# Kernel optimization log

Hardware: AMD Instinct MI355X
Metric: run time of the kernel (lower is better)

## Reference

```python
import jax, jax.numpy as jnp
import numpy as np

B, N, EMB, H = 16, 1024, 128, 8
INNER = EMB * H  # 1024
EPS = 1e-5


def setup_inputs() -> dict:
    key = jax.random.key(0)
    k1, k2, k3 = jax.random.split(key, 3)
    inputs = jax.random.normal(k1, (B, N, EMB), dtype=jnp.float32)
    ln_gamma = jnp.ones((EMB,), dtype=jnp.float32)
    ln_beta = jnp.zeros((EMB,), dtype=jnp.float32)
    w_qkv = jax.random.normal(k2, (EMB, 3 * INNER), dtype=jnp.float32) * (EMB ** -0.5)
    w_proj = jax.random.normal(k3, (INNER, EMB), dtype=jnp.float32) * (INNER ** -0.5)
    b_proj = jnp.zeros((EMB,), dtype=jnp.float32)
    return {"inputs": inputs, "ln_gamma": ln_gamma, "ln_beta": ln_beta,
            "w_qkv": w_qkv, "w_proj": w_proj, "b_proj": b_proj}


def reference(inputs, ln_gamma, ln_beta, w_qkv, w_proj, b_proj):
    scale = INNER ** -0.5
    # LayerNorm over last dim
    mu = jnp.mean(inputs, axis=-1, keepdims=True)
    var = jnp.var(inputs, axis=-1, keepdims=True)
    x = (inputs - mu) * jax.lax.rsqrt(var + EPS) * ln_gamma + ln_beta
    # QKV projection (no bias)
    qkv = x @ w_qkv                                  # [b, n, 3*inner]
    q, k, v = jnp.split(qkv, 3, axis=-1)             # each [b, n, inner]
    def to_heads(a):
        return a.reshape(B, N, H, EMB).transpose(0, 2, 1, 3)  # [b, h, n, d]
    q, k, v = to_heads(q), to_heads(k), to_heads(v)
    attn = jnp.einsum('bhid,bhjd->bhij', q * scale, k)
    attn = jax.nn.softmax(attn, axis=-1)
    out = jnp.einsum('bhij,bhjd->bhid', attn, v)     # [b, h, n, d]
    out = out.transpose(0, 2, 1, 3).reshape(B, N, INNER)
    return out @ w_proj + b_proj                     # [b, n, emb]
```

## Files before the change

### kernel.cpp

```cpp
#include <hip/hip_runtime.h>
#include <hip/hip_bf16.h>


typedef __attribute__((ext_vector_type(8))) short bf16x8;
typedef __attribute__((ext_vector_type(4))) float f32x4;
typedef __attribute__((ext_vector_type(4))) unsigned int u32x4;

__device__ __forceinline__ unsigned short f2bf(float f) {
  unsigned int u = __float_as_uint(f);
  u += 0x7FFF + ((u >> 16) & 1);
  return (unsigned short)(u >> 16);
}

__device__ __forceinline__ void gll16(const void* g, void* l) {
  __builtin_amdgcn_global_load_lds((const __attribute__((address_space(1))) unsigned int*)g,
                                   (__attribute__((address_space(3))) unsigned int*)l, 16, 0, 0);
}

__global__ __launch_bounds__(256) void k_prep(const float* __restrict__ x,
                                              const float* __restrict__ gamma,
                                              const float* __restrict__ beta,
                                              const float* __restrict__ wqkv,
                                              const float* __restrict__ wproj,
                                              unsigned short* __restrict__ xb,
                                              unsigned short* __restrict__ wqkvT,
                                              unsigned short* __restrict__ wprojT) {
  __shared__ unsigned short T[17152];
  const int bid = blockIdx.x, tid = threadIdx.x;
  if (bid < 4096) {
    int row  = bid * 4 + (tid >> 6);
    int lane = tid & 63;
    float2 v = *reinterpret_cast<const float2*>(x + row * 128 + lane * 2);
    float s = v.x + v.y, ss = v.x * v.x + v.y * v.y;
#pragma unroll
    for (int m = 1; m < 64; m <<= 1) { s += __shfl_xor(s, m); ss += __shfl_xor(ss, m); }
    float mu   = s * (1.0f / 128.0f);
    float var  = ss * (1.0f / 128.0f) - mu * mu;
    float rstd = rsqrtf(var + 1e-5f);
    float2 g  = *reinterpret_cast<const float2*>(gamma + lane * 2);
    float2 be = *reinterpret_cast<const float2*>(beta + lane * 2);
    ushort2 o;
    o.x = f2bf((v.x - mu) * rstd * g.x + be.x);
    o.y = f2bf((v.y - mu) * rstd * g.y + be.y);
    *reinterpret_cast<ushort2*>(xb + row * 128 + lane * 2) = o;
  } else if (bid < 4144) {
    const int n0 = (bid - 4096) * 64;
#pragma unroll
    for (int i = 0; i < 32; i++) {
      int idx = i * 256 + tid;
      int k = idx >> 6, c = idx & 63;
      T[k * 70 + c] = f2bf(wqkv[k * 3072 + n0 + c]);
    }
    __syncthreads();
#pragma unroll
    for (int i = 0; i < 32; i++) {
      int idx = i * 256 + tid;
      int n = idx >> 7, k = idx & 127;
      wqkvT[(n0 + n) * 128 + k] = T[k * 70 + n];
    }
  } else {
    const int k0 = (bid - 4144) * 128;
#pragma unroll
    for (int i = 0; i < 64; i++) {
      int idx = i * 256 + tid;
      int r = idx >> 7, c = idx & 127;
      T[r * 134 + c] = f2bf(wproj[(k0 + r) * 128 + c]);
    }
    __syncthreads();
#pragma unroll
    for (int i = 0; i < 64; i++) {
      int idx = i * 256 + tid;
      int c = idx >> 7, r = idx & 127;
      wprojT[c * 1024 + k0 + r] = T[r * 134 + c];
    }
  }
}

__global__ __launch_bounds__(256) void k_qkv(const unsigned short* __restrict__ xb,
                                             const unsigned short* __restrict__ wt,
                                             unsigned short* __restrict__ qb,
                                             unsigned short* __restrict__ kb,
                                             unsigned short* __restrict__ vtb) {
  __shared__ __align__(16) unsigned short SH[24576];
  unsigned short* Xs = SH;
  unsigned short* Ws = SH + 8192;
  const int m0 = blockIdx.x * 64;
  const int n0 = blockIdx.y * 128;
  const int tid = threadIdx.x, wave = tid >> 6, lane = tid & 63;
  const int lm = lane & 15, lg = lane >> 4;
  const int wr = wave >> 1, wc = wave & 1;

#pragma unroll
  for (int ii = 0; ii < 4; ii++) {
    int row = wave * 16 + ii * 4 + (lane >> 4);
    int c = (lane & 15) ^ (row & 7);
    gll16(xb + (m0 + row) * 128 + c * 8, Xs + (wave * 16 + ii * 4) * 128);
  }
#pragma unroll
  for (int ii = 0; ii < 8; ii++) {
    int row = wave * 32 + ii * 4 + (lane >> 4);
    int c = (lane & 15) ^ (row & 7);
    gll16(wt + (n0 + row) * 128 + c * 8, Ws + (wave * 32 + ii * 4) * 128);
  }
  __syncthreads();

  f32x4 acc[2][4];
#pragma unroll
  for (int i = 0; i < 2; i++)
#pragma unroll
    for (int j = 0; j < 4; j++) acc[i][j] = {0.f, 0.f, 0.f, 0.f};

#pragma unroll
  for (int k32 = 0; k32 < 4; k32++) {
    bf16x8 af[2], bfr[4];
#pragma unroll
    for (int mi = 0; mi < 2; mi++) {
      int row = wr * 32 + mi * 16 + lm;
      af[mi] = *(const bf16x8*)((const char*)(Xs + row * 128) + ((k32 * 64 + lg * 16) ^ ((lm & 7) << 4)));
    }
#pragma unroll
    for (int ni = 0; ni < 4; ni++) {
      int row = wc * 64 + ni * 16 + lm;
      bfr[ni] = *(const bf16x8*)((const char*)(Ws + row * 128) + ((k32 * 64 + lg * 16) ^ ((lm & 7) << 4)));
    }
#pragma unroll
    for (int mi = 0; mi < 2; mi++)
#pragma unroll
      for (int ni = 0; ni < 4; ni++)
        acc[mi][ni] = __builtin_amdgcn_mfma_f32_16x16x32_bf16(af[mi], bfr[ni], acc[mi][ni], 0, 0, 0);
  }

  __syncthreads();
  unsigned short* T = SH;
  const int isV = (n0 >= 2048);
  const float qscale = (n0 < 1024) ? 0.04508422f : 1.0f;
#pragma unroll
  for (int mi = 0; mi < 2; mi++)
#pragma unroll
    for (int ni = 0; ni < 4; ni++)
#pragma unroll
      for (int j = 0; j < 4; j++) {
        int mloc = wr * 32 + mi * 16 + 4 * lg + j;
        int nloc = wc * 64 + ni * 16 + lm;
        unsigned short v = f2bf(acc[mi][ni][j] * qscale);
        if (isV) T[nloc * 72 + mloc] = v;
        else     T[mloc * 136 + nloc] = v;
      }
  __syncthreads();
  const int bb = m0 >> 10, seq0 = m0 & 1023;
  const int hh = (n0 & 1023) >> 7;
  const int bh = bb * 8 + hh;
  if (!isV) {
    unsigned short* outp = (n0 < 1024) ? (qb + (bh * 1024 + seq0) * 128)
                                       : (kb + (bh * 1024 + seq0) * 128);
#pragma unroll
    for (int i = 0; i < 16; i++) {
      int flat = i * 512 + tid * 2;
      int row = flat >> 7, c = flat & 127;
      ushort2 v2 = *(ushort2*)&T[row * 136 + c];
      *(ushort2*)(outp + row * 128 + c) = v2;
    }
  } else {
    unsigned short* outp = vtb + bh * 131072 + seq0;
#pragma unroll
    for (int i = 0; i < 16; i++) {
      int flat = i * 512 + tid * 2;
      int row = flat >> 6, c = flat & 63;
      int k = c & 31;
      int p = ((k & 12) << 1) | ((k >> 4) << 2) | (k & 3);
      int cp = (c & 32) | p;
      ushort2 v2 = *(ushort2*)&T[row * 72 + c];
      *(ushort2*)(outp + row * 1024 + cp) = v2;
    }
  }
}

__global__ __launch_bounds__(256, 3) void k_flash(const unsigned short* __restrict__ qb,
                                                  const unsigned short* __restrict__ kb,
                                                  const unsigned short* __restrict__ vtb,
                                                  unsigned short* __restrict__ ob) {
  __shared__ __align__(16) unsigned short Ks[2][32][128];
  __shared__ __align__(16) unsigned short Vts[2][128][32];
  const int bi = blockIdx.x;
  const int xcd = bi & 7, g = bi >> 3;
  const int bh = xcd + 8 * (g >> 3);
  const int q0 = (g & 7) * 128;
  const int tid = threadIdx.x, wave = tid >> 6, lane = tid & 63;
  const int lm = lane & 15, lg = lane >> 4, lk8 = lg * 8;
  const int sw = (lm & 7) << 4;
  const int pvsw = ((lm >> 1) & 3) << 4;
  const int b = bh >> 3, h = bh & 7;

  const unsigned short* kbh = kb + bh * 131072;
  const unsigned short* vbh = vtb + bh * 131072;

  bf16x8 aq[2][4];
#pragma unroll
  for (int qs = 0; qs < 2; qs++) {
    const unsigned short* qrow = qb + (bh * 1024 + q0 + wave * 32 + qs * 16 + lm) * 128;
#pragma unroll
    for (int kc = 0; kc < 4; kc++) aq[qs][kc] = *(const bf16x8*)(qrow + kc * 32 + lk8);
  }

  f32x4 oacc[2][8];
#pragma unroll
  for (int qs = 0; qs < 2; qs++)
#pragma unroll
    for (int dt = 0; dt < 8; dt++) oacc[qs][dt] = {0.f, 0.f, 0.f, 0.f};
  float mrun[2] = {0.f, 0.f}, lrun[2] = {0.f, 0.f};

  auto stage = [&](int kt, int buf) {
#pragma unroll
    for (int ii = 0; ii < 2; ii++) {
      int krow = wave * 8 + ii * 4 + (lane >> 4);
      int c = (lane & 15) ^ (krow & 7);
      gll16(kbh + (kt * 32 + krow) * 128 + c * 8, &Ks[buf][wave * 8 + ii * 4][0]);
    }
#pragma unroll
    for (int ii = 0; ii < 2; ii++) {
      int vrow = wave * 32 + ii * 16 + (lane >> 2);
      int c = (lane & 3) ^ ((vrow >> 1) & 3);
      gll16(vbh + vrow * 1024 + kt * 32 + c * 8, &Vts[buf][wave * 32 + ii * 16][0]);
    }
  };

  stage(0, 0);
  __syncthreads();
  int cur = 0;

  for (int kt = 0; kt < 32; kt++) {
    if (kt < 31) stage(kt + 1, cur ^ 1);
    __builtin_amdgcn_sched_barrier(0);

    f32x4 sc[2][2];
    __builtin_amdgcn_s_setprio(1);
#pragma unroll
    for (int nt = 0; nt < 2; nt++) {
      f32x4 a0 = {0.f, 0.f, 0.f, 0.f}, a1 = {0.f, 0.f, 0.f, 0.f};
      const char* krowp = (const char*)&Ks[cur][nt * 16 + lm][0];
#pragma unroll
      for (int kc = 0; kc < 4; kc++) {
        bf16x8 ak = *(const bf16x8*)(krowp + ((kc * 64 + lg * 16) ^ sw));
        a0 = __builtin_amdgcn_mfma_f32_16x16x32_bf16(ak, aq[0][kc], a0, 0, 0, 0);
        a1 = __builtin_amdgcn_mfma_f32_16x16x32_bf16(ak, aq[1][kc], a1, 0, 0, 0);
      }
      sc[0][nt] = a0; sc[1][nt] = a1;
    }
    __builtin_amdgcn_s_setprio(0);

    unsigned int pw[2][2][2];
#pragma unroll
    for (int qs = 0; qs < 2; qs++) {
      float mx8 = fmaxf(fmaxf(fmaxf(sc[qs][0][0], sc[qs][0][1]), fmaxf(sc[qs][0][2], sc[qs][0][3])),
                        fmaxf(fmaxf(sc[qs][1][0], sc[qs][1][1]), fmaxf(sc[qs][1][2], sc[qs][1][3])));
      if (!__all(mx8 <= mrun[qs] + 8.f)) {
        float mx = fmaxf(mx8, __shfl_xor(mx8, 16));
        mx = fmaxf(mx, __shfl_xor(mx, 32));
        float mnew = fmaxf(mrun[qs], mx);
        float corr = __builtin_exp2f(mrun[qs] - mnew);
        mrun[qs] = mnew;
        lrun[qs] *= corr;
#pragma unroll
        for (int dt = 0; dt < 8; dt++)
#pragma unroll
          for (int j = 0; j < 4; j++) oacc[qs][dt][j] *= corr;
      }
      float ts = 0.f;
#pragma unroll
      for (int nt = 0; nt < 2; nt++) {
        float e0 = __builtin_exp2f(sc[qs][nt][0] - mrun[qs]);
        float e1 = __builtin_exp2f(sc[qs][nt][1] - mrun[qs]);
        float e2 = __builtin_exp2f(sc[qs][nt][2] - mrun[qs]);
        float e3 = __builtin_exp2f(sc[qs][nt][3] - mrun[qs]);
        ts += (e0 + e1) + (e2 + e3);
        asm("v_cvt_pk_bf16_f32 %0, %1, %2" : "=v"(pw[qs][nt][0]) : "v"(e0), "v"(e1));
        asm("v_cvt_pk_bf16_f32 %0, %1, %2" : "=v"(pw[qs][nt][1]) : "v"(e2), "v"(e3));
      }
      lrun[qs] += ts;
    }

    u32x4 t0 = {pw[0][0][0], pw[0][0][1], pw[0][1][0], pw[0][1][1]};
    u32x4 t1 = {pw[1][0][0], pw[1][0][1], pw[1][1][0], pw[1][1][1]};
    bf16x8 pb0 = *(bf16x8*)&t0;
    bf16x8 pb1 = *(bf16x8*)&t1;

    __builtin_amdgcn_s_setprio(1);
#pragma unroll
    for (int dt = 0; dt < 8; dt++) {
      bf16x8 av = *(const bf16x8*)((const char*)&Vts[cur][dt * 16 + lm][0] + ((lg << 4) ^ pvsw));
      oacc[0][dt] = __builtin_amdgcn_mfma_f32_16x16x32_bf16(av, pb0, oacc[0][dt], 0, 0, 0);
      oacc[1][dt] = __builtin_amdgcn_mfma_f32_16x16x32_bf16(av, pb1, oacc[1][dt], 0, 0, 0);
    }
    __builtin_amdgcn_s_setprio(0);

    __syncthreads();
    cur ^= 1;
  }

#pragma unroll
  for (int qs = 0; qs < 2; qs++) {
    float l = lrun[qs];
    l += __shfl_xor(l, 16);
    l += __shfl_xor(l, 32);
    float inv = 1.0f / l;
    unsigned short* orow = ob + ((b * 1024 + q0 + wave * 32 + qs * 16 + lm) * 8 + h) * 128;
#pragma unroll
    for (int dt = 0; dt < 8; dt++) {
#pragma unroll
      for (int pp = 0; pp < 2; pp++) {
        ushort2 o2;
        o2.x = f2bf(oacc[qs][dt][2 * pp]     * inv);
        o2.y = f2bf(oacc[qs][dt][2 * pp + 1] * inv);
        *(ushort2*)&orow[dt * 16 + 4 * lg + 2 * pp] = o2;
      }
    }
  }
}

__global__ __launch_bounds__(256) void k_proj(const unsigned short* __restrict__ ob,
                                              const unsigned short* __restrict__ wpt,
                                              const float* __restrict__ bproj,
                                              float* __restrict__ out) {
  __shared__ __align__(16) unsigned short Os[2][64][128];
  __shared__ __align__(16) unsigned short Ws2[2][128][128];
  const int m0 = blockIdx.x * 64;
  const int tid = threadIdx.x, wave = tid >> 6, lane = tid & 63;
  const int lm = lane & 15, lg = lane >> 4;
  const int wr = wave >> 1, wc = wave & 1;

  auto stage = [&](int kt, int buf) {
#pragma unroll
    for (int ii = 0; ii < 4; ii++) {
      int row = wave * 16 + ii * 4 + (lane >> 4);
      int c = (lane & 15) ^ (row & 7);
      gll16(ob + (m0 + row) * 1024 + kt * 128 + c * 8, &Os[buf][wave * 16 + ii * 4][0]);
    }
#pragma unroll
    for (int ii = 0; ii < 8; ii++) {
      int row = wave * 32 + ii * 4 + (lane >> 4);
      int c = (lane & 15) ^ (row & 7);
      gll16(wpt + row * 1024 + kt * 128 + c * 8, &Ws2[buf][wave * 32 + ii * 4][0]);
    }
  };

  f32x4 acc[2][4];
#pragma unroll
  for (int i = 0; i < 2; i++)
#pragma unroll
    for (int j = 0; j < 4; j++) acc[i][j] = {0.f, 0.f, 0.f, 0.f};

  stage(0, 0);
  __syncthreads();
  int cur = 0;

  for (int kt = 0; kt < 8; kt++) {
    if (kt < 7) stage(kt + 1, cur ^ 1);
    __builtin_amdgcn_sched_barrier(0);
#pragma unroll
    for (int k32 = 0; k32 < 4; k32++) {
      bf16x8 af[2], bfr[4];
#pragma unroll
      for (int mi = 0; mi < 2; mi++) {
        int row = wr * 32 + mi * 16 + lm;
        af[mi] = *(const bf16x8*)((const char*)&Os[cur][row][0] + ((k32 * 64 + lg * 16) ^ ((lm & 7) << 4)));
      }
#pragma unroll
      for (int ni = 0; ni < 4; ni++) {
        int row = wc * 64 + ni * 16 + lm;
        bfr[ni] = *(const bf16x8*)((const char*)&Ws2[cur][row][0] + ((k32 * 64 + lg * 16) ^ ((lm & 7) << 4)));
      }
#pragma unroll
      for (int mi = 0; mi < 2; mi++)
#pragma unroll
        for (int ni = 0; ni < 4; ni++)
          acc[mi][ni] = __builtin_amdgcn_mfma_f32_16x16x32_bf16(af[mi], bfr[ni], acc[mi][ni], 0, 0, 0);
    }
    __syncthreads();
    cur ^= 1;
  }

#pragma unroll
  for (int mi = 0; mi < 2; mi++)
#pragma unroll
    for (int ni = 0; ni < 4; ni++)
#pragma unroll
      for (int j = 0; j < 4; j++) {
        int m = m0 + wr * 32 + mi * 16 + 4 * (lane >> 4) + j;
        int n = wc * 64 + ni * 16 + lm;
        out[m * 128 + n] = acc[mi][ni][j] + bproj[n];
      }
}

extern "C" void kernel_launch(void* const* d_in, const int* in_sizes, int n_in,
                              void* d_out, int out_size, void* d_ws, size_t ws_size,
                              hipStream_t stream) {
  const float* x     = (const float*)d_in[0];
  const float* gamma = (const float*)d_in[1];
  const float* beta  = (const float*)d_in[2];
  const float* wqkv  = (const float*)d_in[3];
  const float* wproj = (const float*)d_in[4];
  const float* bproj = (const float*)d_in[5];
  float* out = (float*)d_out;

  unsigned short* ws = (unsigned short*)d_ws;
  unsigned short* xb     = ws;
  unsigned short* wqkvT  = xb + 2097152;
  unsigned short* wprojT = wqkvT + 393216;
  unsigned short* qbuf   = wprojT + 131072;
  unsigned short* kbuf   = qbuf + 16777216;
  unsigned short* vtbuf  = kbuf + 16777216;
  unsigned short* obuf   = vtbuf + 16777216;

  hipLaunchKernelGGL(k_prep, dim3(4152),    dim3(256), 0, stream, x, gamma, beta, wqkv, wproj, xb, wqkvT, wprojT);
  hipLaunchKernelGGL(k_qkv,  dim3(256, 24), dim3(256), 0, stream, xb, wqkvT, qbuf, kbuf, vtbuf);
  hipLaunchKernelGGL(k_flash, dim3(1024),   dim3(256), 0, stream, qbuf, kbuf, vtbuf, obuf);
  hipLaunchKernelGGL(k_proj, dim3(256),     dim3(256), 0, stream, obuf, wprojT, bproj, out);
}
```

Measured before the change: 161.0 us.

## Double query rows per flash-attention wave to reuse K/V tiles

Each wave of the flash-attention kernel now handles 64 query rows (four 16-row subtiles) instead of 32, so each block covers 256 queries and the grid halves to 512 blocks. Every K and V tile staged in LDS now feeds twice as many MFMAs, which halves K/V global and LDS traffic per query. QK^T and softmax run in two pairs of subtiles, and the PV step issues four MFMAs per V fragment load. In exchange, accumulator registers double, the occupancy hint of 3 is removed, and 512 blocks may underfill the GPU's compute units.

Measured after the change: 201.9 us. 1.25x slower.

```diff
diff --git a/kernel.cpp b/kernel.cpp
--- a/kernel.cpp
+++ b/kernel.cpp
@@ -175,16 +175,16 @@
   }
 }
 
-__global__ __launch_bounds__(256, 3) void k_flash(const unsigned short* __restrict__ qb,
-                                                  const unsigned short* __restrict__ kb,
-                                                  const unsigned short* __restrict__ vtb,
-                                                  unsigned short* __restrict__ ob) {
+__global__ __launch_bounds__(256) void k_flash(const unsigned short* __restrict__ qb,
+                                               const unsigned short* __restrict__ kb,
+                                               const unsigned short* __restrict__ vtb,
+                                               unsigned short* __restrict__ ob) {
   __shared__ __align__(16) unsigned short Ks[2][32][128];
   __shared__ __align__(16) unsigned short Vts[2][128][32];
   const int bi = blockIdx.x;
   const int xcd = bi & 7, g = bi >> 3;
-  const int bh = xcd + 8 * (g >> 3);
-  const int q0 = (g & 7) * 128;
+  const int bh = xcd + 8 * (g >> 2);
+  const int q0 = (g & 3) * 256;
   const int tid = threadIdx.x, wave = tid >> 6, lane = tid & 63;
   const int lm = lane & 15, lg = lane >> 4, lk8 = lg * 8;
   const int sw = (lm & 7) << 4;
@@ -194,20 +194,21 @@
   const unsigned short* kbh = kb + bh * 131072;
   const unsigned short* vbh = vtb + bh * 131072;
 
-  bf16x8 aq[2][4];
-#pragma unroll
-  for (int qs = 0; qs < 2; qs++) {
-    const unsigned short* qrow = qb + (bh * 1024 + q0 + wave * 32 + qs * 16 + lm) * 128;
+  bf16x8 aq[4][4];
+#pragma unroll
+  for (int qs = 0; qs < 4; qs++) {
+    const unsigned short* qrow = qb + (bh * 1024 + q0 + wave * 64 + qs * 16 + lm) * 128;
 #pragma unroll
     for (int kc = 0; kc < 4; kc++) aq[qs][kc] = *(const bf16x8*)(qrow + kc * 32 + lk8);
   }
 
-  f32x4 oacc[2][8];
-#pragma unroll
-  for (int qs = 0; qs < 2; qs++)
+  f32x4 oacc[4][8];
+#pragma unroll
+  for (int qs = 0; qs < 4; qs++)
 #pragma unroll
     for (int dt = 0; dt < 8; dt++) oacc[qs][dt] = {0.f, 0.f, 0.f, 0.f};
-  float mrun[2] = {0.f, 0.f}, lrun[2] = {0.f, 0.f};
+  float mrun[4] = {0.f, 0.f, 0.f, 0.f};
+  float lrun[4] = {0.f, 0.f, 0.f, 0.f};
 
   auto stage = [&](int kt, int buf) {
 #pragma unroll
@@ -232,64 +233,75 @@
     if (kt < 31) stage(kt + 1, cur ^ 1);
     __builtin_amdgcn_sched_barrier(0);
 
-    f32x4 sc[2][2];
-    __builtin_amdgcn_s_setprio(1);
-#pragma unroll
-    for (int nt = 0; nt < 2; nt++) {
-      f32x4 a0 = {0.f, 0.f, 0.f, 0.f}, a1 = {0.f, 0.f, 0.f, 0.f};
-      const char* krowp = (const char*)&Ks[cur][nt * 16 + lm][0];
-#pragma unroll
-      for (int kc = 0; kc < 4; kc++) {
-        bf16x8 ak = *(const bf16x8*)(krowp + ((kc * 64 + lg * 16) ^ sw));
-        a0 = __builtin_amdgcn_mfma_f32_16x16x32_bf16(ak, aq[0][kc], a0, 0, 0, 0);
-        a1 = __builtin_amdgcn_mfma_f32_16x16x32_bf16(ak, aq[1][kc], a1, 0, 0, 0);
-      }
-      sc[0][nt] = a0; sc[1][nt] = a1;
-    }
-    __builtin_amdgcn_s_setprio(0);
-
-    unsigned int pw[2][2][2];
-#pragma unroll
-    for (int qs = 0; qs < 2; qs++) {
-      float mx8 = fmaxf(fmaxf(fmaxf(sc[qs][0][0], sc[qs][0][1]), fmaxf(sc[qs][0][2], sc[qs][0][3])),
-                        fmaxf(fmaxf(sc[qs][1][0], sc[qs][1][1]), fmaxf(sc[qs][1][2], sc[qs][1][3])));
-      if (!__all(mx8 <= mrun[qs] + 8.f)) {
-        float mx = fmaxf(mx8, __shfl_xor(mx8, 16));
-        mx = fmaxf(mx, __shfl_xor(mx, 32));
-        float mnew = fmaxf(mrun[qs], mx);
-        float corr = __builtin_exp2f(mrun[qs] - mnew);
-        mrun[qs] = mnew;
-        lrun[qs] *= corr;
-#pragma unroll
-        for (int dt = 0; dt < 8; dt++)
-#pragma unroll
-          for (int j = 0; j < 4; j++) oacc[qs][dt][j] *= corr;
-      }
-      float ts = 0.f;
+    unsigned int pw[4][2][2];
+
+#pragma unroll
+    for (int pr = 0; pr < 2; pr++) {
+      f32x4 sc[2][2];
+      __builtin_amdgcn_s_setprio(1);
 #pragma unroll
       for (int nt = 0; nt < 2; nt++) {
-        float e0 = __builtin_exp2f(sc[qs][nt][0] - mrun[qs]);
-        float e1 = __builtin_exp2f(sc[qs][nt][1] - mrun[qs]);
-        float e2 = __builtin_exp2f(sc[qs][nt][2] - mrun[qs]);
-        float e3 = __builtin_exp2f(sc[qs][nt][3] - mrun[qs]);
-        ts += (e0 + e1) + (e2 + e3);
-        asm("v_cvt_pk_bf16_f32 %0, %1, %2" : "=v"(pw[qs][nt][0]) : "v"(e0), "v"(e1));
-        asm("v_cvt_pk_bf16_f32 %0, %1, %2" : "=v"(pw[qs][nt][1]) : "v"(e2), "v"(e3));
-      }
-      lrun[qs] += ts;
-    }
-
-    u32x4 t0 = {pw[0][0][0], pw[0][0][1], pw[0][1][0], pw[0][1][1]};
-    u32x4 t1 = {pw[1][0][0], pw[1][0][1], pw[1][1][0], pw[1][1][1]};
-    bf16x8 pb0 = *(bf16x8*)&t0;
-    bf16x8 pb1 = *(bf16x8*)&t1;
+        const char* krowp = (const char*)&Ks[cur][nt * 16 + lm][0];
+        bf16x8 ak[4];
+#pragma unroll
+        for (int kc = 0; kc < 4; kc++)
+          ak[kc] = *(const bf16x8*)(krowp + ((kc * 64 + lg * 16) ^ sw));
+        f32x4 a0 = {0.f, 0.f, 0.f, 0.f}, a1 = {0.f, 0.f, 0.f, 0.f};
+#pragma unroll
+        for (int kc = 0; kc < 4; kc++) {
+          a0 = __builtin_amdgcn_mfma_f32_16x16x32_bf16(ak[kc], aq[2 * pr][kc], a0, 0, 0, 0);
+          a1 = __builtin_amdgcn_mfma_f32_16x16x32_bf16(ak[kc], aq[2 * pr + 1][kc], a1, 0, 0, 0);
+        }
+        sc[0][nt] = a0; sc[1][nt] = a1;
+      }
+      __builtin_amdgcn_s_setprio(0);
+
+#pragma unroll
+      for (int qq = 0; qq < 2; qq++) {
+        const int qs = 2 * pr + qq;
+        float mx8 = fmaxf(fmaxf(fmaxf(sc[qq][0][0], sc[qq][0][1]), fmaxf(sc[qq][0][2], sc[qq][0][3])),
+                          fmaxf(fmaxf(sc[qq][1][0], sc[qq][1][1]), fmaxf(sc[qq][1][2], sc[qq][1][3])));
+        if (!__all(mx8 <= mrun[qs] + 8.f)) {
+          float mx = fmaxf(mx8, __shfl_xor(mx8, 16));
+          mx = fmaxf(mx, __shfl_xor(mx, 32));
+          float mnew = fmaxf(mrun[qs], mx);
+          float corr = __builtin_exp2f(mrun[qs] - mnew);
+          mrun[qs] = mnew;
+          lrun[qs] *= corr;
+#pragma unroll
+          for (int dt = 0; dt < 8; dt++)
+#pragma unroll
+            for (int j = 0; j < 4; j++) oacc[qs][dt][j] *= corr;
+        }
+        float ts = 0.f;
+#pragma unroll
+        for (int nt = 0; nt < 2; nt++) {
+          float e0 = __builtin_exp2f(sc[qq][nt][0] - mrun[qs]);
+          float e1 = __builtin_exp2f(sc[qq][nt][1] - mrun[qs]);
+          float e2 = __builtin_exp2f(sc[qq][nt][2] - mrun[qs]);
+          float e3 = __builtin_exp2f(sc[qq][nt][3] - mrun[qs]);
+          ts += (e0 + e1) + (e2 + e3);
+          asm("v_cvt_pk_bf16_f32 %0, %1, %2" : "=v"(pw[qs][nt][0]) : "v"(e0), "v"(e1));
+          asm("v_cvt_pk_bf16_f32 %0, %1, %2" : "=v"(pw[qs][nt][1]) : "v"(e2), "v"(e3));
+        }
+        lrun[qs] += ts;
+      }
+    }
+
+    bf16x8 pb[4];
+#pragma unroll
+    for (int qs = 0; qs < 4; qs++) {
+      u32x4 t = {pw[qs][0][0], pw[qs][0][1], pw[qs][1][0], pw[qs][1][1]};
+      pb[qs] = *(bf16x8*)&t;
+    }
 
     __builtin_amdgcn_s_setprio(1);
 #pragma unroll
     for (int dt = 0; dt < 8; dt++) {
       bf16x8 av = *(const bf16x8*)((const char*)&Vts[cur][dt * 16 + lm][0] + ((lg << 4) ^ pvsw));
-      oacc[0][dt] = __builtin_amdgcn_mfma_f32_16x16x32_bf16(av, pb0, oacc[0][dt], 0, 0, 0);
-      oacc[1][dt] = __builtin_amdgcn_mfma_f32_16x16x32_bf16(av, pb1, oacc[1][dt], 0, 0, 0);
+#pragma unroll
+      for (int qs = 0; qs < 4; qs++)
+        oacc[qs][dt] = __builtin_amdgcn_mfma_f32_16x16x32_bf16(av, pb[qs], oacc[qs][dt], 0, 0, 0);
     }
     __builtin_amdgcn_s_setprio(0);
 
@@ -298,12 +310,12 @@
   }
 
 #pragma unroll
-  for (int qs = 0; qs < 2; qs++) {
+  for (int qs = 0; qs < 4; qs++) {
     float l = lrun[qs];
     l += __shfl_xor(l, 16);
     l += __shfl_xor(l, 32);
     float inv = 1.0f / l;
-    unsigned short* orow = ob + ((b * 1024 + q0 + wave * 32 + qs * 16 + lm) * 8 + h) * 128;
+    unsigned short* orow = ob + ((b * 1024 + q0 + wave * 64 + qs * 16 + lm) * 8 + h) * 128;
 #pragma unroll
     for (int dt = 0; dt < 8; dt++) {
 #pragma unroll
@@ -413,6 +425,6 @@
 
   hipLaunchKernelGGL(k_prep, dim3(4152),    dim3(256), 0, stream, x, gamma, beta, wqkv, wproj, xb, wqkvT, wprojT);
   hipLaunchKernelGGL(k_qkv,  dim3(256, 24), dim3(256), 0, stream, xb, wqkvT, qbuf, kbuf, vtbuf);
-  hipLaunchKernelGGL(k_flash, dim3(1024),   dim3(256), 0, stream, qbuf, kbuf, vtbuf, obuf);
+  hipLaunchKernelGGL(k_flash, dim3(512),    dim3(256), 0, stream, qbuf, kbuf, vtbuf, obuf);
   hipLaunchKernelGGL(k_proj, dim3(256),     dim3(256), 0, stream, obuf, wprojT, bproj, out);
 }
```
